# Kernel tuning notes

Measured on AMD Instinct MI355X. Metric: run time of the kernel, lower is better.

Reference implementation:

```python
import jax, jax.numpy as jnp
import numpy as np

HIDDEN = 256

def setup_inputs() -> dict:
    key = jax.random.key(0)
    k1, k2, k3, k4, k5 = jax.random.split(key, 5)
    B, T, I, H = 1024, 336, 64, HIDDEN
    s = 1.0 / np.sqrt(H)  # PyTorch LSTM init scale
    return {
        "x": jax.random.normal(k1, (B, T, I), dtype=jnp.float32),
        "W_ih": jax.random.uniform(k2, (4 * H, I), dtype=jnp.float32, minval=-s, maxval=s),
        "W_hh": jax.random.uniform(k3, (4 * H, H), dtype=jnp.float32, minval=-s, maxval=s),
        "b_ih": jax.random.uniform(k4, (4 * H,), dtype=jnp.float32, minval=-s, maxval=s),
        "b_hh": jax.random.uniform(k5, (4 * H,), dtype=jnp.float32, minval=-s, maxval=s),
    }

def reference(x, W_ih, W_hh, b_ih, b_hh):
    # Single-layer unidirectional LSTM (batch_first), PyTorch gate order i,f,g,o.
    B, T, I = x.shape
    H = W_hh.shape[1]
    # Precompute input contribution for all timesteps: [T, B, 4H]
    x_gates = jnp.einsum('bti,gi->tbg', x, W_ih) + (b_ih + b_hh)

    def step(carry, xg_t):
        h, c = carry
        gates = xg_t + h @ W_hh.T          # [B, 4H]
        i, f, g, o = jnp.split(gates, 4, axis=-1)
        c_new = jax.nn.sigmoid(f) * c + jax.nn.sigmoid(i) * jnp.tanh(g)
        h_new = jax.nn.sigmoid(o) * jnp.tanh(c_new)
        return (h_new, c_new), None

    h0 = jnp.zeros((B, H), dtype=x.dtype)
    c0 = jnp.zeros((B, H), dtype=x.dtype)
    (hT, cT), _ = jax.lax.scan(step, (h0, c0), x_gates)
    # hn, cn shaped [num_layers*D, B, H] = [1, B, H]
    return hT[None], cT[None]
```

## Files before the change

### kernel.cpp

```cpp
#include <hip/hip_runtime.h>
#include <cstdint>


#define NGROUP  64
#define BATCH_G 16
#define T_STEPS 336
#define I_DIM   64
#define H_DIM   256
#define VSTRIDE 336
#define PAIRS   128
#define OUT_HALF 262144

typedef __attribute__((ext_vector_type(8))) __bf16 bf16x8;
typedef __attribute__((ext_vector_type(8))) unsigned short ushort8_t;
typedef __attribute__((ext_vector_type(4))) float f32x4;
typedef __attribute__((ext_vector_type(4))) unsigned uint32x4;
typedef __attribute__((ext_vector_type(2))) unsigned uint32x2;

__device__ inline unsigned short f2bf(float f) {
  unsigned u = __builtin_bit_cast(unsigned, f);
  return (unsigned short)((u + 0x7fffu + ((u >> 16) & 1u)) >> 16);
}
__device__ inline float sigf(float x) { return 1.f / (1.f + __expf(-x)); }
__device__ inline float tanhfast(float x) { return 1.f - 2.f / (1.f + __expf(2.f * x)); }

__device__ inline int slot_kt(int s, int mid) {
  return (s < 2) ? s
       : (s < 4) ? (2 + 2 * mid + (s - 2))
       : (((s - 4) < 2 * mid) ? (s - 2) : s);
}

__device__ inline void ld2_tagged(const uint32x2* p, uint32x4& a, uint32x4& b) {
  asm volatile(
      "global_load_dwordx4 %0, %2, off sc0 sc1\n\t"
      "global_load_dwordx4 %1, %3, off sc0 sc1\n\t"
      "s_waitcnt vmcnt(0)"
      : "=&v"(a), "=&v"(b)
      : "v"(p), "v"(p + 2)
      : "memory");
}
__device__ inline void st_pair(uint32x2* p, uint32x2 v) {
  asm volatile("global_store_dwordx2 %0, %1, off sc0 sc1" :: "v"(p), "v"(v) : "memory");
}

__device__ inline void stage_h(const uint32x2* hsrc, unsigned tag, unsigned short* hdst) {
  uint32x4 A, Bv;
  int it = 0;
  for (;;) {
    ld2_tagged(hsrc, A, Bv);
    bool ok = (A[0] == tag) & (A[2] == tag) & (Bv[0] == tag) & (Bv[2] == tag);
    if (ok) break;
    if (++it > (1 << 17)) break;
    __builtin_amdgcn_s_sleep(1);
  }
  *(unsigned*)(hdst + 0 * VSTRIDE) = A[1];
  *(unsigned*)(hdst + 1 * VSTRIDE) = A[3];
  *(unsigned*)(hdst + 2 * VSTRIDE) = Bv[1];
  *(unsigned*)(hdst + 3 * VSTRIDE) = Bv[3];
}

__global__ __launch_bounds__(512, 2) void lstm_persistent(
    const float* __restrict__ x, const float* __restrict__ W_ih,
    const float* __restrict__ W_hh, const float* __restrict__ b_ih,
    const float* __restrict__ b_hh, float* __restrict__ out,
    uint32x2* __restrict__ hbuf)
{
  __shared__ __align__(16) unsigned short v_lds[2][BATCH_G * VSTRIDE];

  const int tid  = threadIdx.x;
  const int gid  = blockIdx.x & 63;
  const int mid  = blockIdx.x >> 6;
  const int wv   = tid >> 6;
  const int l    = tid & 63;
  const int l15  = l & 15, quad = l >> 4;
  const int rg   = wv;

  bf16x8 afrag[2][10];
#pragma unroll
  for (int rt = 0; rt < 2; ++rt) {
    int grow = (l15 & 3) * H_DIM + mid * 64 + rg * 8 + rt * 4 + (l15 >> 2);
    const float* wih_row = W_ih + (long)grow * I_DIM;
    const float* whh_row = W_hh + (long)grow * H_DIM;
#pragma unroll
    for (int s = 0; s < 10; ++s) {
      int kt = slot_kt(s, mid);
      int kbase = kt * 32 + quad * 8;
      ushort8_t a;
#pragma unroll
      for (int e = 0; e < 8; ++e) {
        int k = kbase + e;
        float v = (k < I_DIM) ? wih_row[k] : whh_row[k - I_DIM];
        a[e] = f2bf(v);
      }
      afrag[rt][s] = __builtin_bit_cast(bf16x8, a);
    }
  }

  f32x4 bias[2];
#pragma unroll
  for (int rt = 0; rt < 2; ++rt) {
#pragma unroll
    for (int g = 0; g < 4; ++g) {
      int grow = g * H_DIM + mid * 64 + rg * 8 + rt * 4 + quad;
      bias[rt][g] = b_ih[grow] + b_hh[grow];
    }
  }

  const int batch = l15;
  float c_reg[2] = {0.f, 0.f};
  float h_keep[2];

  const int b_stage = tid >> 5;
  const int x_i2    = (tid & 31) * 2;
  const float* xrow = x + ((long)(gid * BATCH_G + b_stage)) * T_STEPS * I_DIM + x_i2;

  const int p_ld  = tid >> 2;
  const int b0_ld = (tid & 3) * 4;
  const uint32x2* ld_base = hbuf + ((long)gid * PAIRS + p_ld) * BATCH_G + b0_ld;

  uint32x2* st_base = hbuf + ((long)gid * PAIRS + mid * 32 + rg * 4 + (quad >> 1)) * BATCH_G + batch;
  const long buf_stride = (long)NGROUP * PAIRS * BATCH_G;
  const bool own_wave = ((wv >> 1) == mid);

  {
    int zr = tid >> 5, zc = (tid & 31) * 8;
    uint32x4 z = {0u, 0u, 0u, 0u};
    *(uint32x4*)&v_lds[1][zr * VSTRIDE + I_DIM + zc] = z;
  }

  float2 xv = *(const float2*)xrow;

  for (int t = 1; t <= T_STEPS; ++t) {
    unsigned short* vbuf = v_lds[t & 1];

    {
      ushort2 xb;
      xb.x = f2bf(xv.x); xb.y = f2bf(xv.y);
      *(ushort2*)&vbuf[b_stage * VSTRIDE + x_i2] = xb;
    }
    if (t < T_STEPS) xv = *(const float2*)(xrow + (long)t * I_DIM);

    __syncthreads();

    f32x4 acc0 = bias[0], acc1 = bias[1];
    const unsigned short* vb = vbuf + (unsigned)batch * VSTRIDE + quad * 8;
#pragma unroll
    for (int s = 0; s < 4; ++s) {
      int kt = slot_kt(s, mid);
      bf16x8 bv = __builtin_bit_cast(bf16x8, *(const uint32x4*)(vb + kt * 32));
      acc0 = __builtin_amdgcn_mfma_f32_16x16x32_bf16(afrag[0][s], bv, acc0, 0, 0, 0);
      acc1 = __builtin_amdgcn_mfma_f32_16x16x32_bf16(afrag[1][s], bv, acc1, 0, 0, 0);
    }

    if (t > 1 && !own_wave) {
      unsigned short* hdst = vbuf + b0_ld * VSTRIDE + I_DIM + 2 * p_ld;
      const uint32x2* hsrc = ld_base + ((t - 1) & 1) * buf_stride;
      stage_h(hsrc, (unsigned)(t - 1), hdst);
    }
    __syncthreads();

#pragma unroll
    for (int s = 4; s < 10; ++s) {
      int kt = slot_kt(s, mid);
      bf16x8 bv = __builtin_bit_cast(bf16x8, *(const uint32x4*)(vb + kt * 32));
      acc0 = __builtin_amdgcn_mfma_f32_16x16x32_bf16(afrag[0][s], bv, acc0, 0, 0, 0);
      acc1 = __builtin_amdgcn_mfma_f32_16x16x32_bf16(afrag[1][s], bv, acc1, 0, 0, 0);
    }

    __builtin_amdgcn_s_setprio(1);
    unsigned short* next_own = v_lds[(t + 1) & 1] + batch * VSTRIDE + I_DIM + mid * 64;
#pragma unroll
    for (int rt = 0; rt < 2; ++rt) {
      const f32x4 acc = rt ? acc1 : acc0;
      float c = sigf(acc[1]) * c_reg[rt] + sigf(acc[0]) * tanhfast(acc[2]);
      float h = sigf(acc[3]) * tanhfast(c);
      c_reg[rt] = c; h_keep[rt] = h;
      unsigned short hb16 = f2bf(h);
      next_own[rg * 8 + rt * 4 + quad] = hb16;
      unsigned hb = (unsigned)hb16;
      unsigned partner = (unsigned)__shfl_xor((int)hb, 16, 64);
      if (!(quad & 1)) {
        uint32x2 pv;
        pv[0] = (unsigned)t;
        pv[1] = hb | (partner << 16);
        st_pair(st_base + rt * 2 * BATCH_G + (t & 1) * buf_stride, pv);
      }
    }
    __builtin_amdgcn_s_setprio(0);
  }

#pragma unroll
  for (int rt = 0; rt < 2; ++rt) {
    int gcol = mid * 64 + rg * 8 + rt * 4 + quad;
    long o = (long)(gid * BATCH_G + batch) * H_DIM + gcol;
    out[o]            = h_keep[rt];
    out[OUT_HALF + o] = c_reg[rt];
  }
}

extern "C" void kernel_launch(void* const* d_in, const int* in_sizes, int n_in,
                              void* d_out, int out_size, void* d_ws, size_t ws_size,
                              hipStream_t stream) {
  const float* x    = (const float*)d_in[0];
  const float* W_ih = (const float*)d_in[1];
  const float* W_hh = (const float*)d_in[2];
  const float* b_ih = (const float*)d_in[3];
  const float* b_hh = (const float*)d_in[4];
  float* out = (float*)d_out;

  uint32x2* hbuf = (uint32x2*)d_ws;

  hipMemsetAsync(d_ws, 0, 2u * NGROUP * PAIRS * BATCH_G * 8u, stream);
  lstm_persistent<<<dim3(256), dim3(512), 0, stream>>>(x, W_ih, W_hh, b_ih, b_hh, out, hbuf);
}
```

Before: 789.3 us.

## Split hidden dim across two blocks per 8-batch group instead of four

Regroups work so each group of 8 batch rows is handled by 2 cooperating blocks, each owning 128 hidden units, rather than 4 blocks each owning 64 units for 16 batch rows. Each block now exchanges h with only one partner, issues the tagged global load before the first MFMA batch and polls afterwards, which cuts the inter-block synchronisation fan-in and overlaps the load with compute. The cost is that half of each 16-wide MFMA B tile is wasted on duplicated batch rows, each wave now carries four accumulator tiles, and more register pressure.

```diff
diff --git a/kernel.cpp b/kernel.cpp
--- a/kernel.cpp
+++ b/kernel.cpp
@@ -2,8 +2,8 @@
 #include <cstdint>
 
 
-#define NGROUP  64
-#define BATCH_G 16
+#define NGROUP  128
+#define BATCH_G 8
 #define T_STEPS 336
 #define I_DIM   64
 #define H_DIM   256
@@ -26,37 +26,12 @@
 
 __device__ inline int slot_kt(int s, int mid) {
   return (s < 2) ? s
-       : (s < 4) ? (2 + 2 * mid + (s - 2))
-       : (((s - 4) < 2 * mid) ? (s - 2) : s);
-}
-
-__device__ inline void ld2_tagged(const uint32x2* p, uint32x4& a, uint32x4& b) {
-  asm volatile(
-      "global_load_dwordx4 %0, %2, off sc0 sc1\n\t"
-      "global_load_dwordx4 %1, %3, off sc0 sc1\n\t"
-      "s_waitcnt vmcnt(0)"
-      : "=&v"(a), "=&v"(b)
-      : "v"(p), "v"(p + 2)
-      : "memory");
-}
+       : (s < 6) ? (2 + 4 * mid + (s - 2))
+       : (2 + 4 * (1 - mid) + (s - 6));
+}
+
 __device__ inline void st_pair(uint32x2* p, uint32x2 v) {
   asm volatile("global_store_dwordx2 %0, %1, off sc0 sc1" :: "v"(p), "v"(v) : "memory");
-}
-
-__device__ inline void stage_h(const uint32x2* hsrc, unsigned tag, unsigned short* hdst) {
-  uint32x4 A, Bv;
-  int it = 0;
-  for (;;) {
-    ld2_tagged(hsrc, A, Bv);
-    bool ok = (A[0] == tag) & (A[2] == tag) & (Bv[0] == tag) & (Bv[2] == tag);
-    if (ok) break;
-    if (++it > (1 << 17)) break;
-    __builtin_amdgcn_s_sleep(1);
-  }
-  *(unsigned*)(hdst + 0 * VSTRIDE) = A[1];
-  *(unsigned*)(hdst + 1 * VSTRIDE) = A[3];
-  *(unsigned*)(hdst + 2 * VSTRIDE) = Bv[1];
-  *(unsigned*)(hdst + 3 * VSTRIDE) = Bv[3];
 }
 
 __global__ __launch_bounds__(512, 2) void lstm_persistent(
@@ -68,17 +43,17 @@
   __shared__ __align__(16) unsigned short v_lds[2][BATCH_G * VSTRIDE];
 
   const int tid  = threadIdx.x;
-  const int gid  = blockIdx.x & 63;
-  const int mid  = blockIdx.x >> 6;
+  const int gid  = blockIdx.x & (NGROUP - 1);
+  const int mid  = blockIdx.x >> 7;
   const int wv   = tid >> 6;
   const int l    = tid & 63;
   const int l15  = l & 15, quad = l >> 4;
   const int rg   = wv;
 
-  bf16x8 afrag[2][10];
-#pragma unroll
-  for (int rt = 0; rt < 2; ++rt) {
-    int grow = (l15 & 3) * H_DIM + mid * 64 + rg * 8 + rt * 4 + (l15 >> 2);
+  bf16x8 afrag[4][10];
+#pragma unroll
+  for (int rt = 0; rt < 4; ++rt) {
+    int grow = (l15 & 3) * H_DIM + mid * 128 + rg * 16 + rt * 4 + (l15 >> 2);
     const float* wih_row = W_ih + (long)grow * I_DIM;
     const float* whh_row = W_hh + (long)grow * H_DIM;
 #pragma unroll
@@ -96,105 +71,122 @@
     }
   }
 
-  f32x4 bias[2];
-#pragma unroll
-  for (int rt = 0; rt < 2; ++rt) {
+  f32x4 bias[4];
+#pragma unroll
+  for (int rt = 0; rt < 4; ++rt) {
 #pragma unroll
     for (int g = 0; g < 4; ++g) {
-      int grow = g * H_DIM + mid * 64 + rg * 8 + rt * 4 + quad;
+      int grow = g * H_DIM + mid * 128 + rg * 16 + rt * 4 + quad;
       bias[rt][g] = b_ih[grow] + b_hh[grow];
     }
   }
 
-  const int batch = l15;
-  float c_reg[2] = {0.f, 0.f};
-  float h_keep[2];
-
-  const int b_stage = tid >> 5;
-  const int x_i2    = (tid & 31) * 2;
-  const float* xrow = x + ((long)(gid * BATCH_G + b_stage)) * T_STEPS * I_DIM + x_i2;
-
-  const int p_ld  = tid >> 2;
-  const int b0_ld = (tid & 3) * 4;
-  const uint32x2* ld_base = hbuf + ((long)gid * PAIRS + p_ld) * BATCH_G + b0_ld;
-
-  uint32x2* st_base = hbuf + ((long)gid * PAIRS + mid * 32 + rg * 4 + (quad >> 1)) * BATCH_G + batch;
+  const int  batch = l15;
+  const bool bok   = (l15 < 8);
+  float c_reg[4] = {0.f, 0.f, 0.f, 0.f};
+  float h_keep[4];
+
+  const int b_stage = tid >> 6;
+  const int x_if    = tid & 63;
+  const float* xrow = x + ((long)(gid * BATCH_G + b_stage)) * T_STEPS * I_DIM + x_if;
+
+  const int pair_r   = tid >> 3;
+  const int batch_ld = tid & 7;
+  const uint32x2* ld_src = hbuf + ((long)gid * PAIRS + (1 - mid) * 64 + pair_r) * BATCH_G + batch_ld;
+
+  uint32x2* st_base = hbuf + ((long)gid * PAIRS + mid * 64 + rg * 8 + (quad >> 1)) * BATCH_G + batch;
   const long buf_stride = (long)NGROUP * PAIRS * BATCH_G;
-  const bool own_wave = ((wv >> 1) == mid);
 
   {
-    int zr = tid >> 5, zc = (tid & 31) * 8;
-    uint32x4 z = {0u, 0u, 0u, 0u};
-    *(uint32x4*)&v_lds[1][zr * VSTRIDE + I_DIM + zc] = z;
-  }
-
-  float2 xv = *(const float2*)xrow;
+    int zr = tid >> 6, zc = (tid & 63) * 4;
+    uint32x2 z; z[0] = 0u; z[1] = 0u;
+    *(uint32x2*)&v_lds[1][zr * VSTRIDE + I_DIM + zc] = z;
+  }
+
+  float xv = *xrow;
 
   for (int t = 1; t <= T_STEPS; ++t) {
     unsigned short* vbuf = v_lds[t & 1];
 
-    {
-      ushort2 xb;
-      xb.x = f2bf(xv.x); xb.y = f2bf(xv.y);
-      *(ushort2*)&vbuf[b_stage * VSTRIDE + x_i2] = xb;
-    }
-    if (t < T_STEPS) xv = *(const float2*)(xrow + (long)t * I_DIM);
+    vbuf[b_stage * VSTRIDE + x_if] = f2bf(xv);
+    if (t < T_STEPS) xv = xrow[(long)t * I_DIM];
 
     __syncthreads();
 
-    f32x4 acc0 = bias[0], acc1 = bias[1];
-    const unsigned short* vb = vbuf + (unsigned)batch * VSTRIDE + quad * 8;
-#pragma unroll
-    for (int s = 0; s < 4; ++s) {
+    uint32x2 pl;
+    const uint32x2* hsrc = ld_src + ((t - 1) & 1) * buf_stride;
+    if (t > 1)
+      asm volatile("global_load_dwordx2 %0, %1, off sc0 sc1"
+                   : "=v"(pl) : "v"(hsrc) : "memory");
+
+    f32x4 acc[4] = {bias[0], bias[1], bias[2], bias[3]};
+    const unsigned short* vb = vbuf + (unsigned)(l15 & 7) * VSTRIDE + quad * 8;
+#pragma unroll
+    for (int s = 0; s < 6; ++s) {
       int kt = slot_kt(s, mid);
       bf16x8 bv = __builtin_bit_cast(bf16x8, *(const uint32x4*)(vb + kt * 32));
-      acc0 = __builtin_amdgcn_mfma_f32_16x16x32_bf16(afrag[0][s], bv, acc0, 0, 0, 0);
-      acc1 = __builtin_amdgcn_mfma_f32_16x16x32_bf16(afrag[1][s], bv, acc1, 0, 0, 0);
-    }
-
-    if (t > 1 && !own_wave) {
-      unsigned short* hdst = vbuf + b0_ld * VSTRIDE + I_DIM + 2 * p_ld;
-      const uint32x2* hsrc = ld_base + ((t - 1) & 1) * buf_stride;
-      stage_h(hsrc, (unsigned)(t - 1), hdst);
+#pragma unroll
+      for (int rt = 0; rt < 4; ++rt)
+        acc[rt] = __builtin_amdgcn_mfma_f32_16x16x32_bf16(afrag[rt][s], bv, acc[rt], 0, 0, 0);
+    }
+
+    if (t > 1) {
+      asm volatile("s_waitcnt vmcnt(0)" ::: "memory");
+      __builtin_amdgcn_sched_barrier(0);
+      const unsigned tag = (unsigned)(t - 1);
+      int it = 0;
+      while (pl[0] != tag) {
+        if (++it > (1 << 17)) break;
+        __builtin_amdgcn_s_sleep(1);
+        asm volatile("global_load_dwordx2 %0, %1, off sc0 sc1\n\t"
+                     "s_waitcnt vmcnt(0)"
+                     : "=v"(pl) : "v"(hsrc) : "memory");
+        __builtin_amdgcn_sched_barrier(0);
+      }
+      *(unsigned*)&vbuf[(unsigned)batch_ld * VSTRIDE + I_DIM + (1 - mid) * 128 + 2 * pair_r] = pl[1];
     }
     __syncthreads();
 
 #pragma unroll
-    for (int s = 4; s < 10; ++s) {
+    for (int s = 6; s < 10; ++s) {
       int kt = slot_kt(s, mid);
       bf16x8 bv = __builtin_bit_cast(bf16x8, *(const uint32x4*)(vb + kt * 32));
-      acc0 = __builtin_amdgcn_mfma_f32_16x16x32_bf16(afrag[0][s], bv, acc0, 0, 0, 0);
-      acc1 = __builtin_amdgcn_mfma_f32_16x16x32_bf16(afrag[1][s], bv, acc1, 0, 0, 0);
+#pragma unroll
+      for (int rt = 0; rt < 4; ++rt)
+        acc[rt] = __builtin_amdgcn_mfma_f32_16x16x32_bf16(afrag[rt][s], bv, acc[rt], 0, 0, 0);
     }
 
     __builtin_amdgcn_s_setprio(1);
-    unsigned short* next_own = v_lds[(t + 1) & 1] + batch * VSTRIDE + I_DIM + mid * 64;
-#pragma unroll
-    for (int rt = 0; rt < 2; ++rt) {
-      const f32x4 acc = rt ? acc1 : acc0;
-      float c = sigf(acc[1]) * c_reg[rt] + sigf(acc[0]) * tanhfast(acc[2]);
-      float h = sigf(acc[3]) * tanhfast(c);
-      c_reg[rt] = c; h_keep[rt] = h;
+    unsigned short* next_own = v_lds[(t + 1) & 1] + (unsigned)batch * VSTRIDE + I_DIM + mid * 128;
+#pragma unroll
+    for (int rt = 0; rt < 4; ++rt) {
+      float cc = sigf(acc[rt][1]) * c_reg[rt] + sigf(acc[rt][0]) * tanhfast(acc[rt][2]);
+      float h  = sigf(acc[rt][3]) * tanhfast(cc);
+      c_reg[rt] = cc; h_keep[rt] = h;
       unsigned short hb16 = f2bf(h);
-      next_own[rg * 8 + rt * 4 + quad] = hb16;
       unsigned hb = (unsigned)hb16;
-      unsigned partner = (unsigned)__shfl_xor((int)hb, 16, 64);
-      if (!(quad & 1)) {
-        uint32x2 pv;
-        pv[0] = (unsigned)t;
-        pv[1] = hb | (partner << 16);
-        st_pair(st_base + rt * 2 * BATCH_G + (t & 1) * buf_stride, pv);
+      unsigned prt = (unsigned)__shfl_xor((int)hb, 16, 64);
+      if (bok) {
+        next_own[rg * 16 + rt * 4 + quad] = hb16;
+        if (!(quad & 1)) {
+          uint32x2 pv;
+          pv[0] = (unsigned)t;
+          pv[1] = hb | (prt << 16);
+          st_pair(st_base + rt * 2 * BATCH_G + (t & 1) * buf_stride, pv);
+        }
       }
     }
     __builtin_amdgcn_s_setprio(0);
   }
 
 #pragma unroll
-  for (int rt = 0; rt < 2; ++rt) {
-    int gcol = mid * 64 + rg * 8 + rt * 4 + quad;
-    long o = (long)(gid * BATCH_G + batch) * H_DIM + gcol;
-    out[o]            = h_keep[rt];
-    out[OUT_HALF + o] = c_reg[rt];
+  for (int rt = 0; rt < 4; ++rt) {
+    if (bok) {
+      int gcol = mid * 128 + rg * 16 + rt * 4 + quad;
+      long o = (long)(gid * BATCH_G + batch) * H_DIM + gcol;
+      out[o]            = h_keep[rt];
+      out[OUT_HALF + o] = c_reg[rt];
+    }
   }
 }
 
```

After: 1.009 ms. 27.8% more time.

## Load remote hidden-state fragments directly into registers, dropping LDS staging barrier

Applied to the files above, without the earlier changes.

Each wave now polls and loads the other blocks' tagged h pairs from global memory straight into MFMA B-operand registers, instead of having non-owner waves stage them into LDS followed by a second __syncthreads. LDS now holds only x and the block's own 64 h columns (stride shrunk), and loads are issued early to overlap with the first MFMAs. This removes one block-wide barrier per timestep, but every wave now issues redundant global loads for the same data and spins on each fragment separately, with a smaller timeout valve.

```diff
diff --git a/kernel.cpp b/kernel.cpp
--- a/kernel.cpp
+++ b/kernel.cpp
@@ -7,9 +7,10 @@
 #define T_STEPS 336
 #define I_DIM   64
 #define H_DIM   256
-#define VSTRIDE 336
+#define VSTRIDE 136
 #define PAIRS   128
 #define OUT_HALF 262144
+#define VALVE   (1 << 12)
 
 typedef __attribute__((ext_vector_type(8))) __bf16 bf16x8;
 typedef __attribute__((ext_vector_type(8))) unsigned short ushort8_t;
@@ -30,33 +31,8 @@
        : (((s - 4) < 2 * mid) ? (s - 2) : s);
 }
 
-__device__ inline void ld2_tagged(const uint32x2* p, uint32x4& a, uint32x4& b) {
-  asm volatile(
-      "global_load_dwordx4 %0, %2, off sc0 sc1\n\t"
-      "global_load_dwordx4 %1, %3, off sc0 sc1\n\t"
-      "s_waitcnt vmcnt(0)"
-      : "=&v"(a), "=&v"(b)
-      : "v"(p), "v"(p + 2)
-      : "memory");
-}
 __device__ inline void st_pair(uint32x2* p, uint32x2 v) {
   asm volatile("global_store_dwordx2 %0, %1, off sc0 sc1" :: "v"(p), "v"(v) : "memory");
-}
-
-__device__ inline void stage_h(const uint32x2* hsrc, unsigned tag, unsigned short* hdst) {
-  uint32x4 A, Bv;
-  int it = 0;
-  for (;;) {
-    ld2_tagged(hsrc, A, Bv);
-    bool ok = (A[0] == tag) & (A[2] == tag) & (Bv[0] == tag) & (Bv[2] == tag);
-    if (ok) break;
-    if (++it > (1 << 17)) break;
-    __builtin_amdgcn_s_sleep(1);
-  }
-  *(unsigned*)(hdst + 0 * VSTRIDE) = A[1];
-  *(unsigned*)(hdst + 1 * VSTRIDE) = A[3];
-  *(unsigned*)(hdst + 2 * VSTRIDE) = Bv[1];
-  *(unsigned*)(hdst + 3 * VSTRIDE) = Bv[3];
 }
 
 __global__ __launch_bounds__(512, 2) void lstm_persistent(
@@ -114,18 +90,14 @@
   const int x_i2    = (tid & 31) * 2;
   const float* xrow = x + ((long)(gid * BATCH_G + b_stage)) * T_STEPS * I_DIM + x_i2;
 
-  const int p_ld  = tid >> 2;
-  const int b0_ld = (tid & 3) * 4;
-  const uint32x2* ld_base = hbuf + ((long)gid * PAIRS + p_ld) * BATCH_G + b0_ld;
+  const uint32x2* rbase0 = hbuf + (long)gid * PAIRS * BATCH_G + batch;
 
   uint32x2* st_base = hbuf + ((long)gid * PAIRS + mid * 32 + rg * 4 + (quad >> 1)) * BATCH_G + batch;
   const long buf_stride = (long)NGROUP * PAIRS * BATCH_G;
-  const bool own_wave = ((wv >> 1) == mid);
 
   {
-    int zr = tid >> 5, zc = (tid & 31) * 8;
-    uint32x4 z = {0u, 0u, 0u, 0u};
-    *(uint32x4*)&v_lds[1][zr * VSTRIDE + I_DIM + zc] = z;
+    int zr = tid >> 5, zc = (tid & 31) * 2;
+    *(unsigned*)&v_lds[1][zr * VSTRIDE + I_DIM + zc] = 0u;
   }
 
   float2 xv = *(const float2*)xrow;
@@ -145,30 +117,66 @@
     f32x4 acc0 = bias[0], acc1 = bias[1];
     const unsigned short* vb = vbuf + (unsigned)batch * VSTRIDE + quad * 8;
 #pragma unroll
-    for (int s = 0; s < 4; ++s) {
-      int kt = slot_kt(s, mid);
-      bf16x8 bv = __builtin_bit_cast(bf16x8, *(const uint32x4*)(vb + kt * 32));
+    for (int s = 0; s < 2; ++s) {
+      bf16x8 bv = __builtin_bit_cast(bf16x8, *(const uint32x4*)(vb + s * 32));
       acc0 = __builtin_amdgcn_mfma_f32_16x16x32_bf16(afrag[0][s], bv, acc0, 0, 0, 0);
       acc1 = __builtin_amdgcn_mfma_f32_16x16x32_bf16(afrag[1][s], bv, acc1, 0, 0, 0);
     }
 
-    if (t > 1 && !own_wave) {
-      unsigned short* hdst = vbuf + b0_ld * VSTRIDE + I_DIM + 2 * p_ld;
-      const uint32x2* hsrc = ld_base + ((t - 1) & 1) * buf_stride;
-      stage_h(hsrc, (unsigned)(t - 1), hdst);
-    }
-    __syncthreads();
-
-#pragma unroll
-    for (int s = 4; s < 10; ++s) {
-      int kt = slot_kt(s, mid);
-      bf16x8 bv = __builtin_bit_cast(bf16x8, *(const uint32x4*)(vb + kt * 32));
+    uint32x2 rr[6][4];
+    const uint32x2* rb = rbase0 + ((t - 1) & 1) * buf_stride;
+#pragma unroll
+    for (int f = 0; f < 6; ++f) {
+      int kt = slot_kt(4 + f, mid);
+      const uint32x2* pf = rb + ((kt - 2) * 16 + quad * 4) * BATCH_G;
+      asm volatile(
+          "global_load_dwordx2 %0, %4, off sc0 sc1\n\t"
+          "global_load_dwordx2 %1, %4, off offset:128 sc0 sc1\n\t"
+          "global_load_dwordx2 %2, %4, off offset:256 sc0 sc1\n\t"
+          "global_load_dwordx2 %3, %4, off offset:384 sc0 sc1"
+          : "=&v"(rr[f][0]), "=&v"(rr[f][1]), "=&v"(rr[f][2]), "=&v"(rr[f][3])
+          : "v"(pf) : "memory");
+    }
+
+#pragma unroll
+    for (int s = 2; s < 4; ++s) {
+      bf16x8 bv = __builtin_bit_cast(bf16x8, *(const uint32x4*)(vb + s * 32));
       acc0 = __builtin_amdgcn_mfma_f32_16x16x32_bf16(afrag[0][s], bv, acc0, 0, 0, 0);
       acc1 = __builtin_amdgcn_mfma_f32_16x16x32_bf16(afrag[1][s], bv, acc1, 0, 0, 0);
     }
 
+    const unsigned tag = (unsigned)(t - 1);
+#pragma unroll
+    for (int f = 0; f < 6; ++f) {
+      asm volatile("s_waitcnt vmcnt(0)"
+                   : "+v"(rr[f][0]), "+v"(rr[f][1]), "+v"(rr[f][2]), "+v"(rr[f][3])
+                   :: "memory");
+      int it = 0;
+      while (!((rr[f][0][0] == tag) & (rr[f][1][0] == tag) &
+               (rr[f][2][0] == tag) & (rr[f][3][0] == tag))) {
+        if (++it > VALVE) break;
+        __builtin_amdgcn_s_sleep(1);
+        int kt = slot_kt(4 + f, mid);
+        const uint32x2* pf = rb + ((kt - 2) * 16 + quad * 4) * BATCH_G;
+        asm volatile(
+            "global_load_dwordx2 %0, %4, off sc0 sc1\n\t"
+            "global_load_dwordx2 %1, %4, off offset:128 sc0 sc1\n\t"
+            "global_load_dwordx2 %2, %4, off offset:256 sc0 sc1\n\t"
+            "global_load_dwordx2 %3, %4, off offset:384 sc0 sc1\n\t"
+            "s_waitcnt vmcnt(0)"
+            : "=&v"(rr[f][0]), "=&v"(rr[f][1]), "=&v"(rr[f][2]), "=&v"(rr[f][3])
+            : "v"(pf) : "memory");
+      }
+      uint32x4 dw;
+      dw[0] = rr[f][0][1]; dw[1] = rr[f][1][1];
+      dw[2] = rr[f][2][1]; dw[3] = rr[f][3][1];
+      bf16x8 bv = __builtin_bit_cast(bf16x8, dw);
+      acc0 = __builtin_amdgcn_mfma_f32_16x16x32_bf16(afrag[0][4 + f], bv, acc0, 0, 0, 0);
+      acc1 = __builtin_amdgcn_mfma_f32_16x16x32_bf16(afrag[1][4 + f], bv, acc1, 0, 0, 0);
+    }
+
     __builtin_amdgcn_s_setprio(1);
-    unsigned short* next_own = v_lds[(t + 1) & 1] + batch * VSTRIDE + I_DIM + mid * 64;
+    unsigned short* next_own = v_lds[(t + 1) & 1] + (unsigned)batch * VSTRIDE + I_DIM;
 #pragma unroll
     for (int rt = 0; rt < 2; ++rt) {
       const f32x4 acc = rt ? acc1 : acc0;
```

Result: slower. 1.057 ms (+33.9%).
